# Kernel optimization log

Measured on AMD Instinct MI355X. Metric: run time of the kernel, lower is better.

Reference implementation:

```python
import jax, jax.numpy as jnp
import numpy as np

COS_EPS = 1e-8  # torch.nn.CosineSimilarity default eps
B, L, D = 32, 512, 1024
S, E = 256, 64
POS = 17


def _padded_idxs(key, batch, max_len, seq_len, min_frac=0.5):
    """Random first-subword indices in [1, seq_len) with trailing zero padding."""
    k1, k2 = jax.random.split(key)
    lens = jax.random.randint(k1, (batch,), int(max_len * min_frac), max_len + 1)
    vals = jax.random.randint(k2, (batch, max_len), 1, seq_len)
    col = jnp.arange(max_len)[None, :]
    return jnp.where(col < lens[:, None], vals, 0).astype(jnp.int32)


def setup_inputs() -> dict:
    key = jax.random.key(0)
    ks = jax.random.split(key, 7)
    all_embeddings = jax.random.normal(ks[0], (B, L, D), dtype=jnp.float32)
    W = jax.random.uniform(ks[1], (D, D), dtype=jnp.float32) / np.sqrt(D)
    lin_w = jax.random.normal(ks[2], (2, 2 * D + POS), dtype=jnp.float32) * 0.02
    lin_b = jnp.zeros((2,), dtype=jnp.float32)
    idxs_to_collect_sent = _padded_idxs(ks[3], B, S, L)
    idxs_to_collect_event = _padded_idxs(ks[4], B, E, L)
    pos_tag = jax.random.randint(ks[5], (B, S), -1, POS - 1).astype(jnp.int32)
    return {
        "all_embeddings": all_embeddings,
        "W": W,
        "lin_w": lin_w,
        "lin_b": lin_b,
        "idxs_to_collect_sent": idxs_to_collect_sent,
        "idxs_to_collect_event": idxs_to_collect_event,
        "pos_tag": pos_tag,
    }


def _gather_pad(all_embeddings, idxs):
    # idxs has valid (>0) entries at the front, zeros as trailing pad, so the
    # per-sample compact-gather-then-pad loop is equivalent to gather + mask.
    mask = (idxs > 0)  # [B, T]
    gathered = jnp.take_along_axis(
        all_embeddings, jnp.maximum(idxs, 0)[..., None], axis=1)  # [B, T, D]
    return gathered * mask[..., None].astype(all_embeddings.dtype), mask


def reference(all_embeddings, W, lin_w, lin_b,
              idxs_to_collect_sent, idxs_to_collect_event, pos_tag):
    sent, _ = _gather_pad(all_embeddings, idxs_to_collect_sent)       # [B,S,D]
    event, ev_mask = _gather_pad(all_embeddings, idxs_to_collect_event)  # [B,E,D]

    # map_numerator = 1 / number of valid event tokens per sample
    map_num = 1.0 / jnp.sum(ev_mask, axis=-1).astype(sent.dtype)  # [B]

    # cosine similarity between (sent @ W) and event embeddings
    a = jnp.einsum('bsd,de->bse', sent, W)                 # [B,S,D]
    num = jnp.einsum('bsd,bed->bse', a, event)             # [B,S,E]
    na = jnp.maximum(jnp.linalg.norm(a, axis=-1), COS_EPS)       # [B,S]
    ne = jnp.maximum(jnp.linalg.norm(event, axis=-1), COS_EPS)   # [B,E]
    logits = num / (na[:, :, None] * ne[:, None, :])       # [B,S,E]

    sent2event_att = jnp.einsum('bse,bed->bsd', logits, event) * map_num[:, None, None]

    pos = jnp.where(pos_tag < 0, POS - 1, pos_tag)
    pos_oh = jax.nn.one_hot(pos, POS, dtype=sent.dtype)    # [B,S,17]

    feat = jnp.concatenate([sent, sent2event_att, pos_oh], axis=-1)  # [B,S,2D+17]
    return feat @ lin_w.T + lin_b                           # [B,S,2]
```

## Files before the change

### kernel.cpp

```cpp
#include <hip/hip_runtime.h>

#define B_ 32
#define L_ 512
#define D_ 1024
#define S_ 256
#define E_ 64
#define POS_ 17
#define LWS 2065
#define M_ (B_*S_)

typedef __attribute__((ext_vector_type(8))) short short8v;
typedef __attribute__((ext_vector_type(4))) float f32x4;
typedef __attribute__((ext_vector_type(4))) unsigned short us4;

__device__ __forceinline__ unsigned short f2bf(float x) {
  union { float f; unsigned u; } v; v.f = x;
  unsigned r = v.u + 0x7FFFu + ((v.u >> 16) & 1u);
  return (unsigned short)(r >> 16);
}
__device__ __forceinline__ float bf2f(unsigned short b) {
  union { unsigned u; float f; } v; v.u = ((unsigned)b) << 16;
  return v.f;
}
__device__ __forceinline__ void async16(void* lds, const void* g) {
  __builtin_amdgcn_global_load_lds(
      (const __attribute__((address_space(1))) unsigned int*)(unsigned long long)g,
      (__attribute__((address_space(3))) unsigned int*)(unsigned int)(unsigned long long)lds,
      16, 0, 0);
}

__global__ __launch_bounds__(256) void prep_all(
    const float* __restrict__ emb, const float* __restrict__ W,
    const float* __restrict__ lin_w, const float* __restrict__ lin_b,
    const int* __restrict__ idx_s, const int* __restrict__ idx_e,
    const int* __restrict__ pos_tag,
    unsigned short* __restrict__ sentb, unsigned short* __restrict__ evb,
    unsigned short* __restrict__ Wt,
    float* __restrict__ base, float* __restrict__ ne, float* __restrict__ evw) {
  __shared__ float tile[32][33];
  __shared__ float red[12];
  int bid = blockIdx.x;
  int t = threadIdx.x;
  int lane = t & 63, w = t >> 6;

  if (bid >= 10240) {
    int tt = bid - 10240;
    int bx = tt & 31, by = tt >> 5;
    int tx = t & 31, ty = t >> 5;
#pragma unroll
    for (int i = 0; i < 4; i++)
      tile[ty + i * 8][tx] = W[(size_t)(by * 32 + ty + i * 8) * D_ + bx * 32 + tx];
    __syncthreads();
#pragma unroll
    for (int i = 0; i < 4; i++)
      Wt[(size_t)(bx * 32 + ty + i * 8) * D_ + by * 32 + tx] = f2bf(tile[tx][ty + i * 8]);
    return;
  }

  bool is_sent = bid < M_;
  int row = is_sent ? bid : bid - M_;
  int b = is_sent ? (row >> 8) : (row >> 6);
  int idx = is_sent ? idx_s[row] : idx_e[row];
  float msk = idx > 0 ? 1.0f : 0.0f;
  const float* src = emb + ((size_t)b * L_ + (idx > 0 ? idx : 0)) * D_;
  float4 v = *(const float4*)(src + t * 4);
  v.x *= msk; v.y *= msk; v.z *= msk; v.w *= msk;
  us4 o; o.x = f2bf(v.x); o.y = f2bf(v.y); o.z = f2bf(v.z); o.w = f2bf(v.w);
  int d = t * 4;

  if (is_sent) {
    *(us4*)&sentb[(size_t)row * D_ + d] = o;
    const float* lw0 = lin_w;
    const float* lw1 = lin_w + LWS;
    float l0 = v.x * lw0[d] + v.y * lw0[d + 1] + v.z * lw0[d + 2] + v.w * lw0[d + 3];
    float l1 = v.x * lw1[d] + v.y * lw1[d + 1] + v.z * lw1[d + 2] + v.w * lw1[d + 3];
#pragma unroll
    for (int off = 32; off; off >>= 1) {
      l0 += __shfl_xor(l0, off);
      l1 += __shfl_xor(l1, off);
    }
    if (lane == 0) { red[w * 2] = l0; red[w * 2 + 1] = l1; }
    __syncthreads();
    if (t == 0) {
      float L0 = red[0] + red[2] + red[4] + red[6];
      float L1 = red[1] + red[3] + red[5] + red[7];
      int p = pos_tag[row]; if (p < 0) p = POS_ - 1;
      base[(size_t)row * 2 + 0] = L0 + lin_b[0] + lin_w[2 * D_ + p];
      base[(size_t)row * 2 + 1] = L1 + lin_b[1] + lin_w[LWS + 2 * D_ + p];
    }
  } else {
    *(us4*)&evb[(size_t)row * D_ + d] = o;
    const float* lw0 = lin_w + D_;
    const float* lw1 = lin_w + LWS + D_;
    float sq = v.x * v.x + v.y * v.y + v.z * v.z + v.w * v.w;
    float e0 = v.x * lw0[d] + v.y * lw0[d + 1] + v.z * lw0[d + 2] + v.w * lw0[d + 3];
    float e1 = v.x * lw1[d] + v.y * lw1[d + 1] + v.z * lw1[d + 2] + v.w * lw1[d + 3];
#pragma unroll
    for (int off = 32; off; off >>= 1) {
      sq += __shfl_xor(sq, off);
      e0 += __shfl_xor(e0, off);
      e1 += __shfl_xor(e1, off);
    }
    if (lane == 0) { red[w * 3] = sq; red[w * 3 + 1] = e0; red[w * 3 + 2] = e1; }
    __syncthreads();
    if (t == 0) {
      float SQ = red[0] + red[3] + red[6] + red[9];
      float E0 = red[1] + red[4] + red[7] + red[10];
      float E1 = red[2] + red[5] + red[8] + red[11];
      ne[row] = fmaxf(sqrtf(SQ), 1e-8f);
      evw[(size_t)row * 2 + 0] = E0;
      evw[(size_t)row * 2 + 1] = E1;
    }
  }
}

__device__ __forceinline__ void stage_g(const char* gA, const char* gB,
    unsigned short* bA, unsigned short* bB, int t, int kt) {
  int sc = ((t & 7) ^ ((t >> 3) & 7)) << 4;
#pragma unroll
  for (int i = 0; i < 4; i++) {
    int row = i * 32 + (t >> 3);
    size_t src = (size_t)row * (D_ * 2) + (size_t)kt * 128 + sc;
    async16((char*)bA + i * 4096 + t * 16, gA + src);
    async16((char*)bB + i * 4096 + t * 16, gB + src);
  }
}
__device__ __forceinline__ void comp_g(const unsigned short* bA,
    const unsigned short* bB, f32x4 (&acc)[4][4], int wr, int wc, int fr, int hi) {
  int x = fr & 7;
#pragma unroll
  for (int ks = 0; ks < 2; ks++) {
    int co = ((ks * 4 + hi) ^ x) << 3;
    short8v a[4], bv[4];
#pragma unroll
    for (int m = 0; m < 4; m++)
      a[m] = *(const short8v*)&bA[(wr * 64 + m * 16 + fr) * 64 + co];
#pragma unroll
    for (int n = 0; n < 4; n++)
      bv[n] = *(const short8v*)&bB[(wc * 64 + n * 16 + fr) * 64 + co];
#pragma unroll
    for (int m = 0; m < 4; m++)
#pragma unroll
      for (int n = 0; n < 4; n++)
        acc[m][n] = __builtin_amdgcn_mfma_f32_16x16x32_bf16(a[m], bv[n], acc[m][n], 0, 0, 0);
  }
}

__global__ __launch_bounds__(256) void gemm_aw(
    const unsigned short* __restrict__ A,
    const unsigned short* __restrict__ Bt,
    unsigned short* __restrict__ C) {
  const int K = D_, N = D_;
  __shared__ unsigned short sA0[128 * 64], sA1[128 * 64];
  __shared__ unsigned short sB0[128 * 64], sB1[128 * 64];
  int t = threadIdx.x;
  int w = t >> 6, lane = t & 63;
  int wr = w >> 1, wc = w & 1;
  int fr = lane & 15, hi = lane >> 4;
  int n0 = blockIdx.x * 128, m0 = blockIdx.y * 128;
  f32x4 acc[4][4];
#pragma unroll
  for (int m = 0; m < 4; m++)
#pragma unroll
    for (int n = 0; n < 4; n++) acc[m][n] = f32x4{0.f, 0.f, 0.f, 0.f};

  const char* gA = (const char*)(A + (size_t)m0 * K);
  const char* gB = (const char*)(Bt + (size_t)n0 * K);

  stage_g(gA, gB, sA0, sB0, t, 0);
  __syncthreads();
#pragma unroll 1
  for (int kt = 0; kt < 16; kt += 2) {
    stage_g(gA, gB, sA1, sB1, t, kt + 1);
    comp_g(sA0, sB0, acc, wr, wc, fr, hi);
    __syncthreads();
    if (kt + 2 < 16) stage_g(gA, gB, sA0, sB0, t, kt + 2);
    comp_g(sA1, sB1, acc, wr, wc, fr, hi);
    __syncthreads();
  }
#pragma unroll
  for (int m = 0; m < 4; m++) {
#pragma unroll
    for (int r = 0; r < 4; r++) {
      int row = wr * 64 + m * 16 + hi * 4 + r;
      size_t gbase = (size_t)(m0 + row) * N + n0 + wc * 64;
#pragma unroll
      for (int n = 0; n < 4; n++)
        C[gbase + n * 16 + fr] = f2bf(acc[m][n][r]);
    }
  }
}

__device__ __forceinline__ void stage_a(const char* gA, const char* gE,
    unsigned short* bA, unsigned short* bE, int t, int kt) {
  int sc = ((t & 7) ^ ((t >> 3) & 7)) << 4;
#pragma unroll
  for (int i = 0; i < 2; i++) {
    int row = i * 32 + (t >> 3);
    size_t src = (size_t)row * (D_ * 2) + (size_t)kt * 128 + sc;
    async16((char*)bA + i * 4096 + t * 16, gA + src);
    async16((char*)bE + i * 4096 + t * 16, gE + src);
  }
}
__device__ __forceinline__ void comp_a(const unsigned short* bA,
    const unsigned short* bE, f32x4 (&acc)[4], float& rsq, int w, int fr, int hi) {
  int x = fr & 7;
#pragma unroll
  for (int ks = 0; ks < 2; ks++) {
    int co = ((ks * 4 + hi) ^ x) << 3;
    short8v af = *(const short8v*)&bA[(w * 16 + fr) * 64 + co];
#pragma unroll
    for (int j = 0; j < 8; j++) { float xv = bf2f((unsigned short)af[j]); rsq += xv * xv; }
#pragma unroll
    for (int n = 0; n < 4; n++) {
      short8v bv = *(const short8v*)&bE[(n * 16 + fr) * 64 + co];
      acc[n] = __builtin_amdgcn_mfma_f32_16x16x32_bf16(af, bv, acc[n], 0, 0, 0);
    }
  }
}

__global__ __launch_bounds__(256) void attn_ep(
    const unsigned short* __restrict__ Abf,
    const unsigned short* __restrict__ Ebf,
    const int* __restrict__ idx_e,
    const float* __restrict__ ne, const float* __restrict__ evw,
    const float* __restrict__ base,
    float* __restrict__ out) {
  int b = blockIdx.x >> 2;
  int s0 = (blockIdx.x & 3) * 64;
  __shared__ unsigned short sA0[64 * 64], sA1[64 * 64];
  __shared__ unsigned short sE0[64 * 64], sE1[64 * 64];
  __shared__ float sRne[E_], sEvw[E_][2], sRna[64];
  __shared__ float sMapn;
  int t = threadIdx.x;
  int w = t >> 6, lane = t & 63;
  int fr = lane & 15, hi = lane >> 4;
  if (t < E_) {
    sRne[t] = 1.0f / ne[b * E_ + t];
    sEvw[t][0] = evw[(size_t)(b * E_ + t) * 2 + 0];
    sEvw[t][1] = evw[(size_t)(b * E_ + t) * 2 + 1];
    unsigned long long mball = __ballot(idx_e[b * E_ + t] > 0);
    if (t == 0) sMapn = 1.0f / (float)__popcll(mball);
  }
  f32x4 acc[4];
#pragma unroll
  for (int n = 0; n < 4; n++) acc[n] = f32x4{0.f, 0.f, 0.f, 0.f};
  float rsq = 0.f;

  const char* gA = (const char*)(Abf + ((size_t)b * S_ + s0) * D_);
  const char* gE = (const char*)(Ebf + (size_t)b * E_ * D_);

  stage_a(gA, gE, sA0, sE0, t, 0);
  __syncthreads();
#pragma unroll 1
  for (int kt = 0; kt < 16; kt += 2) {
    stage_a(gA, gE, sA1, sE1, t, kt + 1);
    comp_a(sA0, sE0, acc, rsq, w, fr, hi);
    __syncthreads();
    if (kt + 2 < 16) stage_a(gA, gE, sA0, sE0, t, kt + 2);
    comp_a(sA1, sE1, acc, rsq, w, fr, hi);
    __syncthreads();
  }
  rsq += __shfl_xor(rsq, 16);
  rsq += __shfl_xor(rsq, 32);
  if (lane < 16) sRna[w * 16 + lane] = 1.0f / fmaxf(sqrtf(rsq), 1e-8f);
  __syncthreads();

  float mapn = sMapn;
#pragma unroll
  for (int r = 0; r < 4; r++) {
    int srl = w * 16 + hi * 4 + r;
    float rna = sRna[srl];
    float a0 = 0.f, a1 = 0.f;
#pragma unroll
    for (int n = 0; n < 4; n++) {
      int e = n * 16 + fr;
      float lg = acc[n][r] * rna * sRne[e];
      a0 += lg * sEvw[e][0];
      a1 += lg * sEvw[e][1];
    }
#pragma unroll
    for (int off = 1; off < 16; off <<= 1) {
      a0 += __shfl_xor(a0, off);
      a1 += __shfl_xor(a1, off);
    }
    if (fr == 0) {
      size_t sg = (size_t)b * S_ + s0 + srl;
      float2 res;
      res.x = base[sg * 2 + 0] + mapn * a0;
      res.y = base[sg * 2 + 1] + mapn * a1;
      *(float2*)&out[sg * 2] = res;
    }
  }
}

extern "C" void kernel_launch(void* const* d_in, const int* in_sizes, int n_in,
                              void* d_out, int out_size, void* d_ws, size_t ws_size,
                              hipStream_t stream) {
  const float* emb   = (const float*)d_in[0];
  const float* W     = (const float*)d_in[1];
  const float* lin_w = (const float*)d_in[2];
  const float* lin_b = (const float*)d_in[3];
  const int* idx_s   = (const int*)d_in[4];
  const int* idx_e   = (const int*)d_in[5];
  const int* pos     = (const int*)d_in[6];
  float* out = (float*)d_out;

  char* ws = (char*)d_ws;
  const size_t MB = 1024 * 1024;
  unsigned short* sentb = (unsigned short*)(ws);
  unsigned short* abf   = (unsigned short*)(ws + 16 * MB);
  unsigned short* evb   = (unsigned short*)(ws + 32 * MB);
  unsigned short* Wt    = (unsigned short*)(ws + 36 * MB);
  float* ne   = (float*)(ws + 38 * MB);
  float* evw  = ne + 2048;
  float* base = evw + 4096;

  prep_all<<<M_ + B_ * E_ + 1024, 256, 0, stream>>>(
      emb, W, lin_w, lin_b, idx_s, idx_e, pos, sentb, evb, Wt, base, ne, evw);
  gemm_aw<<<dim3(8, 64), 256, 0, stream>>>(sentb, Wt, abf);
  attn_ep<<<B_ * 4, 256, 0, stream>>>(abf, evb, idx_e, ne, evw, base, out);
}
```

Baseline: 52.31 us.

## Use 32x32 MFMA in GEMM, remap blocks, split attention tiles over more blocks

The sent@W GEMM switches from 16x16x32 to 32x32x16 bf16 MFMA with a 2x2 accumulator per wave. This halves the LDS fragment loads per MFMA. Its grid becomes 1D with a remapped block order that places the 8 N-tiles of an M-row on different XCDs. The attention/epilogue kernel now handles 32 rows per block instead of 64 and splits the event dimension across wave pairs, combining partial sums through shared memory. The goal is to double the block count and improve occupancy, at the cost of an extra sync and reloading event tiles per block.

```diff
diff --git a/kernel.cpp b/kernel.cpp
--- a/kernel.cpp
+++ b/kernel.cpp
@@ -11,6 +11,7 @@
 
 typedef __attribute__((ext_vector_type(8))) short short8v;
 typedef __attribute__((ext_vector_type(4))) float f32x4;
+typedef __attribute__((ext_vector_type(16))) float f32x16;
 typedef __attribute__((ext_vector_type(4))) unsigned short us4;
 
 __device__ __forceinline__ unsigned short f2bf(float x) {
@@ -126,23 +127,23 @@
   }
 }
 __device__ __forceinline__ void comp_g(const unsigned short* bA,
-    const unsigned short* bB, f32x4 (&acc)[4][4], int wr, int wc, int fr, int hi) {
-  int x = fr & 7;
-#pragma unroll
-  for (int ks = 0; ks < 2; ks++) {
-    int co = ((ks * 4 + hi) ^ x) << 3;
-    short8v a[4], bv[4];
-#pragma unroll
-    for (int m = 0; m < 4; m++)
-      a[m] = *(const short8v*)&bA[(wr * 64 + m * 16 + fr) * 64 + co];
-#pragma unroll
-    for (int n = 0; n < 4; n++)
-      bv[n] = *(const short8v*)&bB[(wc * 64 + n * 16 + fr) * 64 + co];
-#pragma unroll
-    for (int m = 0; m < 4; m++)
-#pragma unroll
-      for (int n = 0; n < 4; n++)
-        acc[m][n] = __builtin_amdgcn_mfma_f32_16x16x32_bf16(a[m], bv[n], acc[m][n], 0, 0, 0);
+    const unsigned short* bB, f32x16 (&acc)[2][2], int wr, int wc, int fr32, int hi1) {
+  int x = fr32 & 7;
+#pragma unroll
+  for (int ks = 0; ks < 4; ks++) {
+    int co = ((ks * 2 + hi1) ^ x) << 3;
+    short8v a[2], bv[2];
+#pragma unroll
+    for (int m = 0; m < 2; m++)
+      a[m] = *(const short8v*)&bA[(wr * 64 + m * 32 + fr32) * 64 + co];
+#pragma unroll
+    for (int n = 0; n < 2; n++)
+      bv[n] = *(const short8v*)&bB[(wc * 64 + n * 32 + fr32) * 64 + co];
+#pragma unroll
+    for (int m = 0; m < 2; m++)
+#pragma unroll
+      for (int n = 0; n < 2; n++)
+        acc[m][n] = __builtin_amdgcn_mfma_f32_32x32x16_bf16(a[m], bv[n], acc[m][n], 0, 0, 0);
   }
 }
 
@@ -156,13 +157,17 @@
   int t = threadIdx.x;
   int w = t >> 6, lane = t & 63;
   int wr = w >> 1, wc = w & 1;
-  int fr = lane & 15, hi = lane >> 4;
-  int n0 = blockIdx.x * 128, m0 = blockIdx.y * 128;
-  f32x4 acc[4][4];
-#pragma unroll
-  for (int m = 0; m < 4; m++)
-#pragma unroll
-    for (int n = 0; n < 4; n++) acc[m][n] = f32x4{0.f, 0.f, 0.f, 0.f};
+  int fr32 = lane & 31, hi1 = lane >> 5;
+  int bid = blockIdx.x;
+  int wg = ((bid & 7) << 6) | (bid >> 3);
+  int n0 = (wg & 7) * 128, m0 = (wg >> 3) * 128;
+  f32x16 acc[2][2];
+#pragma unroll
+  for (int m = 0; m < 2; m++)
+#pragma unroll
+    for (int n = 0; n < 2; n++)
+#pragma unroll
+      for (int r = 0; r < 16; r++) acc[m][n][r] = 0.f;
 
   const char* gA = (const char*)(A + (size_t)m0 * K);
   const char* gB = (const char*)(Bt + (size_t)n0 * K);
@@ -172,21 +177,22 @@
 #pragma unroll 1
   for (int kt = 0; kt < 16; kt += 2) {
     stage_g(gA, gB, sA1, sB1, t, kt + 1);
-    comp_g(sA0, sB0, acc, wr, wc, fr, hi);
+    comp_g(sA0, sB0, acc, wr, wc, fr32, hi1);
     __syncthreads();
     if (kt + 2 < 16) stage_g(gA, gB, sA0, sB0, t, kt + 2);
-    comp_g(sA1, sB1, acc, wr, wc, fr, hi);
-    __syncthreads();
-  }
-#pragma unroll
-  for (int m = 0; m < 4; m++) {
-#pragma unroll
-    for (int r = 0; r < 4; r++) {
-      int row = wr * 64 + m * 16 + hi * 4 + r;
-      size_t gbase = (size_t)(m0 + row) * N + n0 + wc * 64;
-#pragma unroll
-      for (int n = 0; n < 4; n++)
-        C[gbase + n * 16 + fr] = f2bf(acc[m][n][r]);
+    comp_g(sA1, sB1, acc, wr, wc, fr32, hi1);
+    __syncthreads();
+  }
+#pragma unroll
+  for (int m = 0; m < 2; m++) {
+#pragma unroll
+    for (int n = 0; n < 2; n++) {
+#pragma unroll
+      for (int r = 0; r < 16; r++) {
+        int crow = (r & 3) + 8 * (r >> 2) + 4 * hi1;
+        int row = wr * 64 + m * 32 + crow;
+        C[(size_t)(m0 + row) * N + n0 + wc * 64 + n * 32 + fr32] = f2bf(acc[m][n][r]);
+      }
     }
   }
 }
@@ -194,26 +200,30 @@
 __device__ __forceinline__ void stage_a(const char* gA, const char* gE,
     unsigned short* bA, unsigned short* bE, int t, int kt) {
   int sc = ((t & 7) ^ ((t >> 3) & 7)) << 4;
+  int row = t >> 3;
+  async16((char*)bA + t * 16, gA + (size_t)row * (D_ * 2) + (size_t)kt * 128 + sc);
 #pragma unroll
   for (int i = 0; i < 2; i++) {
-    int row = i * 32 + (t >> 3);
-    size_t src = (size_t)row * (D_ * 2) + (size_t)kt * 128 + sc;
-    async16((char*)bA + i * 4096 + t * 16, gA + src);
-    async16((char*)bE + i * 4096 + t * 16, gE + src);
+    int er = i * 32 + row;
+    async16((char*)bE + i * 4096 + t * 16, gE + (size_t)er * (D_ * 2) + (size_t)kt * 128 + sc);
   }
 }
 __device__ __forceinline__ void comp_a(const unsigned short* bA,
-    const unsigned short* bE, f32x4 (&acc)[4], float& rsq, int w, int fr, int hi) {
+    const unsigned short* bE, f32x4 (&acc)[2], float& rsq, int w, int fr, int hi) {
   int x = fr & 7;
+  int rowA = (w >> 1) * 16 + fr;
+  int ch = w & 1;
 #pragma unroll
   for (int ks = 0; ks < 2; ks++) {
     int co = ((ks * 4 + hi) ^ x) << 3;
-    short8v af = *(const short8v*)&bA[(w * 16 + fr) * 64 + co];
-#pragma unroll
-    for (int j = 0; j < 8; j++) { float xv = bf2f((unsigned short)af[j]); rsq += xv * xv; }
-#pragma unroll
-    for (int n = 0; n < 4; n++) {
-      short8v bv = *(const short8v*)&bE[(n * 16 + fr) * 64 + co];
+    short8v af = *(const short8v*)&bA[rowA * 64 + co];
+    if (ch == 0) {
+#pragma unroll
+      for (int j = 0; j < 8; j++) { float xv = bf2f((unsigned short)af[j]); rsq += xv * xv; }
+    }
+#pragma unroll
+    for (int n = 0; n < 2; n++) {
+      short8v bv = *(const short8v*)&bE[(ch * 32 + n * 16 + fr) * 64 + co];
       acc[n] = __builtin_amdgcn_mfma_f32_16x16x32_bf16(af, bv, acc[n], 0, 0, 0);
     }
   }
@@ -226,11 +236,11 @@
     const float* __restrict__ ne, const float* __restrict__ evw,
     const float* __restrict__ base,
     float* __restrict__ out) {
-  int b = blockIdx.x >> 2;
-  int s0 = (blockIdx.x & 3) * 64;
-  __shared__ unsigned short sA0[64 * 64], sA1[64 * 64];
+  int b = blockIdx.x >> 3;
+  int s0 = (blockIdx.x & 7) * 32;
+  __shared__ unsigned short sA0[32 * 64], sA1[32 * 64];
   __shared__ unsigned short sE0[64 * 64], sE1[64 * 64];
-  __shared__ float sRne[E_], sEvw[E_][2], sRna[64];
+  __shared__ float sRne[E_], sEvw[E_][2], sRna[32], sP[2][32][2];
   __shared__ float sMapn;
   int t = threadIdx.x;
   int w = t >> 6, lane = t & 63;
@@ -242,9 +252,9 @@
     unsigned long long mball = __ballot(idx_e[b * E_ + t] > 0);
     if (t == 0) sMapn = 1.0f / (float)__popcll(mball);
   }
-  f32x4 acc[4];
-#pragma unroll
-  for (int n = 0; n < 4; n++) acc[n] = f32x4{0.f, 0.f, 0.f, 0.f};
+  f32x4 acc[2];
+#pragma unroll
+  for (int n = 0; n < 2; n++) acc[n] = f32x4{0.f, 0.f, 0.f, 0.f};
   float rsq = 0.f;
 
   const char* gA = (const char*)(Abf + ((size_t)b * S_ + s0) * D_);
@@ -263,18 +273,19 @@
   }
   rsq += __shfl_xor(rsq, 16);
   rsq += __shfl_xor(rsq, 32);
-  if (lane < 16) sRna[w * 16 + lane] = 1.0f / fmaxf(sqrtf(rsq), 1e-8f);
+  if ((w & 1) == 0 && lane < 16)
+    sRna[(w >> 1) * 16 + lane] = 1.0f / fmaxf(sqrtf(rsq), 1e-8f);
   __syncthreads();
 
-  float mapn = sMapn;
+  int ch = w & 1;
 #pragma unroll
   for (int r = 0; r < 4; r++) {
-    int srl = w * 16 + hi * 4 + r;
+    int srl = (w >> 1) * 16 + hi * 4 + r;
     float rna = sRna[srl];
     float a0 = 0.f, a1 = 0.f;
 #pragma unroll
-    for (int n = 0; n < 4; n++) {
-      int e = n * 16 + fr;
+    for (int n = 0; n < 2; n++) {
+      int e = ch * 32 + n * 16 + fr;
       float lg = acc[n][r] * rna * sRne[e];
       a0 += lg * sEvw[e][0];
       a1 += lg * sEvw[e][1];
@@ -284,13 +295,14 @@
       a0 += __shfl_xor(a0, off);
       a1 += __shfl_xor(a1, off);
     }
-    if (fr == 0) {
-      size_t sg = (size_t)b * S_ + s0 + srl;
-      float2 res;
-      res.x = base[sg * 2 + 0] + mapn * a0;
-      res.y = base[sg * 2 + 1] + mapn * a1;
-      *(float2*)&out[sg * 2] = res;
-    }
+    if (fr == 0) { sP[ch][srl][0] = a0; sP[ch][srl][1] = a1; }
+  }
+  __syncthreads();
+  if (t < 64) {
+    int row = t >> 1, c = t & 1;
+    float v = sP[0][row][c] + sP[1][row][c];
+    size_t sg = (size_t)b * S_ + s0 + row;
+    out[sg * 2 + c] = base[sg * 2 + c] + sMapn * v;
   }
 }
 
@@ -318,6 +330,6 @@
 
   prep_all<<<M_ + B_ * E_ + 1024, 256, 0, stream>>>(
       emb, W, lin_w, lin_b, idx_s, idx_e, pos, sentb, evb, Wt, base, ne, evw);
-  gemm_aw<<<dim3(8, 64), 256, 0, stream>>>(sentb, Wt, abf);
-  attn_ep<<<B_ * 4, 256, 0, stream>>>(abf, evb, idx_e, ne, evw, base, out);
-}
+  gemm_aw<<<512, 256, 0, stream>>>(sentb, Wt, abf);
+  attn_ep<<<B_ * 8, 256, 0, stream>>>(abf, evb, idx_e, ne, evw, base, out);
+}
```

Measured after the change: 48.26 us. 1.08x faster.
